# Kernel optimization log

Measured on AMD Instinct MI355X. Metric: run time of the kernel, lower is better.

The kernel has to match this reference:

```python
import jax, jax.numpy as jnp
import numpy as np

KSIZE = 3  # kernel_size (stride=1, dilation=1, groups=1, reduction_ratio=1)
BN_EPS = 1e-3  # keras BatchNormalization default epsilon


def setup_inputs() -> dict:
    key = jax.random.key(0)
    k0, k1, k2 = jax.random.split(key, 3)
    B, H, W, C = 8, 128, 128, 64
    x = jax.random.normal(k0, (B, H, W, C), jnp.float32)
    w1 = jax.random.normal(k1, (C, C), jnp.float32) * 0.05      # 1x1 conv C -> C//rr
    b1 = jnp.zeros((C,), jnp.float32)
    gamma = jnp.ones((C,), jnp.float32)
    beta = jnp.zeros((C,), jnp.float32)
    bn_mean = jnp.zeros((C,), jnp.float32)
    bn_var = jnp.ones((C,), jnp.float32)
    w2 = jax.random.normal(k2, (C, KSIZE * KSIZE), jnp.float32) * 0.05  # 1x1 conv -> K*K*G
    b2 = jnp.zeros((KSIZE * KSIZE,), jnp.float32)
    return dict(x=x, w1=w1, b1=b1, gamma=gamma, beta=beta,
                bn_mean=bn_mean, bn_var=bn_var, w2=w2, b2=b2)


def _extract_patches(x, k):
    # tf.image.extract_patches, SAME padding, stride 1, rate 1.
    # Returns (B, H, W, k*k, C) with patch index row-major over (di, dj).
    B, H, W, C = x.shape
    pad = k - 1
    pt = pad // 2
    xp = jnp.pad(x, ((0, 0), (pt, pad - pt), (pt, pad - pt), (0, 0)))
    shifts = [xp[:, i:i + H, j:j + W, :] for i in range(k) for j in range(k)]
    return jnp.stack(shifts, axis=3)


def reference(x, w1, b1, gamma, beta, bn_mean, bn_var, w2, b2):
    B, H, W, C = x.shape
    # kernel generation: 1x1 conv -> BN (inference stats) -> ReLU -> 1x1 conv
    h = jnp.einsum('bhwc,cd->bhwd', x, w1) + b1
    h = (h - bn_mean) * jax.lax.rsqrt(bn_var + BN_EPS) * gamma + beta
    h = jax.nn.relu(h)
    kern = jnp.einsum('bhwc,ck->bhwk', h, w2) + b2        # (B,H,W,K*K)
    # patch extraction + spatially-varying multiply-reduce over K*K
    patches = _extract_patches(x, KSIZE)                   # (B,H,W,K*K,C)
    out = jnp.einsum('bhwkc,bhwk->bhwc', patches, kern)    # (B,H,W,C)
    kernel = kern[..., None, None]                         # (B,H,W,K*K,1,G=1) as in tf reshape
    return out, kernel
```

## Files before the change

kernel.cpp:

```cpp
#include <hip/hip_runtime.h>

typedef unsigned int uint;
typedef unsigned short ushort_t;
typedef __attribute__((ext_vector_type(8))) short short8v;
typedef __attribute__((ext_vector_type(4))) float f32x4;

#define BATCH 8
#define HH 128
#define WW 128
#define CC 64
#define NPIX (BATCH * HH * WW)
#define KK 9
#define BN_EPS 1e-3f

__device__ __forceinline__ uint f2bfbits(float f) {
    uint u = __float_as_uint(f);
    return (u + 0x7fffu + ((u >> 16) & 1u)) >> 16;
}
__device__ __forceinline__ float bflo(uint u) { return __uint_as_float(u << 16); }
__device__ __forceinline__ float bfhi(uint u) { return __uint_as_float(u & 0xffff0000u); }

__global__ void setup_kernel(const float* __restrict__ w1,
                             const float* __restrict__ b1,
                             const float* __restrict__ gamma,
                             const float* __restrict__ beta,
                             const float* __restrict__ bn_mean,
                             const float* __restrict__ bn_var,
                             const float* __restrict__ w2,
                             const float* __restrict__ b2,
                             ushort_t* __restrict__ w1b,
                             ushort_t* __restrict__ w2bT,
                             float* __restrict__ scalef,
                             float* __restrict__ biasf,
                             float* __restrict__ b2f)
{
    int t = blockIdx.x * blockDim.x + threadIdx.x;
    int nt = gridDim.x * blockDim.x;
    for (int idx = t; idx < CC * CC; idx += nt) {
        int d = idx >> 6, c = idx & 63;
        w1b[idx] = (ushort_t)f2bfbits(w1[c * CC + d]);
    }
    for (int idx = t; idx < 16 * CC; idx += nt) {
        int k = idx >> 6, d = idx & 63;
        w2bT[idx] = (k < KK) ? (ushort_t)f2bfbits(w2[d * KK + k]) : (ushort_t)0;
    }
    if (t < CC) {
        float s = gamma[t] * rsqrtf(bn_var[t] + BN_EPS);
        scalef[t] = s;
        biasf[t] = (b1[t] - bn_mean[t]) * s + beta[t];
    }
    if (t < KK) b2f[t] = b2[t];
}

__global__ __launch_bounds__(256) void invol_fused(
    const float* __restrict__ x,
    const ushort_t* __restrict__ w1b,
    const ushort_t* __restrict__ w2bT,
    const float* __restrict__ scalef,
    const float* __restrict__ biasf,
    const float* __restrict__ b2f,
    float* __restrict__ out,
    float* __restrict__ kout)
{
    __shared__ ushort_t xrow[3][66][72];
    __shared__ ushort_t w1L[64][72];
    __shared__ ushort_t w2L[16][72];
    __shared__ ushort_t hL[4][16][72];
    __shared__ float    kS[64][12];

    const int t = threadIdx.x;
    const int w = __builtin_amdgcn_readfirstlane(t >> 6);
    const int l = t & 63;
    const int lq = l >> 4, lr = l & 15;
    int bid = blockIdx.x;
    bid = (bid & 7) * 256 + (bid >> 3);
    const int p0 = bid * 64;

    const int b  = p0 >> 14;
    const int i  = (p0 >> 7) & 127;
    const int j0 = p0 & 127;

#pragma unroll
    for (int r = 0; r < 3; ++r) {
        const int ir = min(max(i + r - 1, 0), HH - 1);
        const float* rowp = x + ((size_t)b * HH + ir) * WW * CC;
#pragma unroll
        for (int s = 0; s < 4; ++s) {
            int u = t + s * 256;
            int slot = u >> 4, c4 = u & 15;
            int jj = min(max(j0 + slot - 1, 0), WW - 1);
            float4 v = *(const float4*)(rowp + (size_t)jj * CC + c4 * 4);
            uint2 pk;
            pk.x = f2bfbits(v.x) | (f2bfbits(v.y) << 16);
            pk.y = f2bfbits(v.z) | (f2bfbits(v.w) << 16);
            *(uint2*)(&xrow[r][slot][c4 * 4]) = pk;
        }
        if (t < 32) {
            int u = t + 1024;
            int slot = u >> 4, c4 = u & 15;
            int jj = min(max(j0 + slot - 1, 0), WW - 1);
            float4 v = *(const float4*)(rowp + (size_t)jj * CC + c4 * 4);
            uint2 pk;
            pk.x = f2bfbits(v.x) | (f2bfbits(v.y) << 16);
            pk.y = f2bfbits(v.z) | (f2bfbits(v.w) << 16);
            *(uint2*)(&xrow[r][slot][c4 * 4]) = pk;
        }
    }
#pragma unroll
    for (int s = 0; s < 2; ++s) {
        int u = t + s * 256;
        int row = u >> 3, seg = u & 7;
        uint4 v = *(const uint4*)(w1b + row * CC + seg * 8);
        *(uint4*)(&w1L[row][seg * 8]) = v;
    }
    if (t < 128) {
        int row = t >> 3, seg = t & 7;
        uint4 v = *(const uint4*)(w2bT + row * CC + seg * 8);
        *(uint4*)(&w2L[row][seg * 8]) = v;
    }
    __syncthreads();

    {
        short8v af[2];
#pragma unroll
        for (int ks = 0; ks < 2; ++ks)
            af[ks] = *(const short8v*)(&xrow[1][w * 16 + lr + 1][ks * 32 + lq * 8]);

        f32x4 acc[4];
#pragma unroll
        for (int n = 0; n < 4; ++n) acc[n] = (f32x4){0.f, 0.f, 0.f, 0.f};
#pragma unroll
        for (int ks = 0; ks < 2; ++ks)
#pragma unroll
            for (int n = 0; n < 4; ++n) {
                short8v bf = *(const short8v*)(&w1L[n * 16 + lr][ks * 32 + lq * 8]);
                acc[n] = __builtin_amdgcn_mfma_f32_16x16x32_bf16(af[ks], bf, acc[n], 0, 0, 0);
            }
#pragma unroll
        for (int n = 0; n < 4; ++n) {
            const int d = n * 16 + lr;
            const float s = scalef[d], bb = biasf[d];
#pragma unroll
            for (int r = 0; r < 4; ++r) {
                float hv = fmaxf(fmaf(acc[n][r], s, bb), 0.f);
                hL[w][lq * 4 + r][d] = (ushort_t)f2bfbits(hv);
            }
        }
    }

    {
        f32x4 acc2 = (f32x4){0.f, 0.f, 0.f, 0.f};
#pragma unroll
        for (int ks = 0; ks < 2; ++ks) {
            short8v a2  = *(const short8v*)(&hL[w][lr][ks * 32 + lq * 8]);
            short8v b2v = *(const short8v*)(&w2L[lr][ks * 32 + lq * 8]);
            acc2 = __builtin_amdgcn_mfma_f32_16x16x32_bf16(a2, b2v, acc2, 0, 0, 0);
        }
        if (lr < KK) {
            const float bk = b2f[lr];
#pragma unroll
            for (int r = 0; r < 4; ++r)
                kS[w * 16 + lq * 4 + r][lr] = acc2[r] + bk;
        }
    }
    {
        float* kbase = kout + (size_t)(p0 + w * 16) * KK;
        if (l < 36) {
            float v[4];
#pragma unroll
            for (int e = 0; e < 4; ++e) {
                int f = l * 4 + e;
                v[e] = kS[w * 16 + f / KK][f % KK];
            }
            *(f32x4*)(kbase + l * 4) = (f32x4){v[0], v[1], v[2], v[3]};
        }
    }

    {
        float* obase = out + (size_t)(p0 + w * 16) * CC;
#pragma unroll
        for (int r = 0; r < 4; ++r) {
            const int flat = r * 64 + l;
            const int pxo = flat >> 4;
            const int g = flat & 15;
            const int pix = w * 16 + pxo;
            float a0 = 0.f, a1 = 0.f, a2 = 0.f, a3 = 0.f;
#pragma unroll
            for (int ti = 0; ti < 3; ++ti) {
                const int ii = i + ti - 1;
                if (ii < 0 || ii >= HH) continue;
#pragma unroll
                for (int tj = 0; tj < 3; ++tj) {
                    int jj = j0 + pix + tj - 1;
                    bool valid = (jj >= 0) && (jj < WW);
                    float kv = valid ? kS[pix][ti * 3 + tj] : 0.f;
                    uint2 u = *(const uint2*)(&xrow[ti][pix + tj][g * 4]);
                    a0 = fmaf(kv, bflo(u.x), a0);
                    a1 = fmaf(kv, bfhi(u.x), a1);
                    a2 = fmaf(kv, bflo(u.y), a2);
                    a3 = fmaf(kv, bfhi(u.y), a3);
                }
            }
            *(f32x4*)(obase + (size_t)flat * 4) = (f32x4){a0, a1, a2, a3};
        }
    }
}

extern "C" void kernel_launch(void* const* d_in, const int* in_sizes, int n_in,
                              void* d_out, int out_size, void* d_ws, size_t ws_size,
                              hipStream_t stream) {
    const float* x       = (const float*)d_in[0];
    const float* w1      = (const float*)d_in[1];
    const float* b1      = (const float*)d_in[2];
    const float* gamma   = (const float*)d_in[3];
    const float* beta    = (const float*)d_in[4];
    const float* bn_mean = (const float*)d_in[5];
    const float* bn_var  = (const float*)d_in[6];
    const float* w2      = (const float*)d_in[7];
    const float* b2      = (const float*)d_in[8];

    ushort_t* w1b  = (ushort_t*)d_ws;
    ushort_t* w2bT = w1b + CC * CC;
    float* scalef  = (float*)(w2bT + 16 * CC);
    float* biasf   = scalef + CC;
    float* b2f     = biasf + CC;

    float* out  = (float*)d_out;
    float* kout = out + (size_t)NPIX * CC;

    hipLaunchKernelGGL(setup_kernel, dim3(20), dim3(256), 0, stream,
                       w1, b1, gamma, beta, bn_mean, bn_var, w2, b2,
                       w1b, w2bT, scalef, biasf, b2f);

    hipLaunchKernelGGL(invol_fused, dim3(NPIX / 64), dim3(256), 0, stream,
                       x, w1b, w2bT, scalef, biasf, b2f, out, kout);
}
```

Before: 31.93 us.

## Process four rows per block with LDS row ring buffer and register prefetch

```diff
diff --git a/kernel.cpp b/kernel.cpp
--- a/kernel.cpp
+++ b/kernel.cpp
@@ -12,6 +12,8 @@
 #define NPIX (BATCH * HH * WW)
 #define KK 9
 #define BN_EPS 1e-3f
+#define ROWS 4
+#define NBLK (NPIX / (64 * ROWS))
 
 __device__ __forceinline__ uint f2bfbits(float f) {
     uint u = __float_as_uint(f);
@@ -62,7 +64,7 @@
     float* __restrict__ out,
     float* __restrict__ kout)
 {
-    __shared__ ushort_t xrow[3][66][72];
+    __shared__ ushort_t xrow[4][66][72];
     __shared__ ushort_t w1L[64][72];
     __shared__ ushort_t w2L[16][72];
     __shared__ ushort_t hL[4][16][72];
@@ -73,37 +75,56 @@
     const int l = t & 63;
     const int lq = l >> 4, lr = l & 15;
     int bid = blockIdx.x;
-    bid = (bid & 7) * 256 + (bid >> 3);
-    const int p0 = bid * 64;
-
-    const int b  = p0 >> 14;
-    const int i  = (p0 >> 7) & 127;
-    const int j0 = p0 & 127;
-
-#pragma unroll
-    for (int r = 0; r < 3; ++r) {
-        const int ir = min(max(i + r - 1, 0), HH - 1);
-        const float* rowp = x + ((size_t)b * HH + ir) * WW * CC;
+    bid = (bid & 7) * (NBLK / 8) + (bid >> 3);
+
+    const int jhalf = bid & 1;
+    const int grp = (bid >> 1) & 31;
+    const int b = bid >> 6;
+    const int i0 = grp * ROWS;
+    const int j0 = jhalf * 64;
+
+    auto stage_row_to_regs = [&](int ro, float4* sv) {
+        const float* rowp = x + ((size_t)b * HH + min(max(ro, 0), HH - 1)) * WW * CC;
 #pragma unroll
         for (int s = 0; s < 4; ++s) {
             int u = t + s * 256;
             int slot = u >> 4, c4 = u & 15;
             int jj = min(max(j0 + slot - 1, 0), WW - 1);
-            float4 v = *(const float4*)(rowp + (size_t)jj * CC + c4 * 4);
-            uint2 pk;
-            pk.x = f2bfbits(v.x) | (f2bfbits(v.y) << 16);
-            pk.y = f2bfbits(v.z) | (f2bfbits(v.w) << 16);
-            *(uint2*)(&xrow[r][slot][c4 * 4]) = pk;
+            sv[s] = *(const float4*)(rowp + (size_t)jj * CC + c4 * 4);
         }
         if (t < 32) {
             int u = t + 1024;
             int slot = u >> 4, c4 = u & 15;
             int jj = min(max(j0 + slot - 1, 0), WW - 1);
-            float4 v = *(const float4*)(rowp + (size_t)jj * CC + c4 * 4);
+            sv[4] = *(const float4*)(rowp + (size_t)jj * CC + c4 * 4);
+        }
+    };
+    auto write_row_to_lds = [&](int ringslot, const float4* sv) {
+#pragma unroll
+        for (int s = 0; s < 4; ++s) {
+            int u = t + s * 256;
+            int slot = u >> 4, c4 = u & 15;
             uint2 pk;
-            pk.x = f2bfbits(v.x) | (f2bfbits(v.y) << 16);
-            pk.y = f2bfbits(v.z) | (f2bfbits(v.w) << 16);
-            *(uint2*)(&xrow[r][slot][c4 * 4]) = pk;
+            pk.x = f2bfbits(sv[s].x) | (f2bfbits(sv[s].y) << 16);
+            pk.y = f2bfbits(sv[s].z) | (f2bfbits(sv[s].w) << 16);
+            *(uint2*)(&xrow[ringslot][slot][c4 * 4]) = pk;
+        }
+        if (t < 32) {
+            int u = t + 1024;
+            int slot = u >> 4, c4 = u & 15;
+            uint2 pk;
+            pk.x = f2bfbits(sv[4].x) | (f2bfbits(sv[4].y) << 16);
+            pk.y = f2bfbits(sv[4].z) | (f2bfbits(sv[4].w) << 16);
+            *(uint2*)(&xrow[ringslot][slot][c4 * 4]) = pk;
+        }
+    };
+
+    {
+        float4 sv[5];
+#pragma unroll
+        for (int r = 0; r < 3; ++r) {
+            stage_row_to_regs(i0 - 1 + r, sv);
+            write_row_to_lds(r, sv);
         }
     }
 #pragma unroll
@@ -120,88 +141,104 @@
     }
     __syncthreads();
 
-    {
-        short8v af[2];
-#pragma unroll
-        for (int ks = 0; ks < 2; ++ks)
-            af[ks] = *(const short8v*)(&xrow[1][w * 16 + lr + 1][ks * 32 + lq * 8]);
-
-        f32x4 acc[4];
-#pragma unroll
-        for (int n = 0; n < 4; ++n) acc[n] = (f32x4){0.f, 0.f, 0.f, 0.f};
-#pragma unroll
-        for (int ks = 0; ks < 2; ++ks)
+#pragma unroll
+    for (int r = 0; r < ROWS; ++r) {
+        const int i = i0 + r;
+        const int p0 = ((b * HH + i) * WW) + j0;
+        const int sTop = r & 3, sMid = (r + 1) & 3, sBot = (r + 2) & 3, sNew = (r + 3) & 3;
+
+        float4 sv[5];
+        if (r < ROWS - 1) stage_row_to_regs(i0 + r + 2, sv);
+
+        {
+            short8v af[2];
+#pragma unroll
+            for (int ks = 0; ks < 2; ++ks)
+                af[ks] = *(const short8v*)(&xrow[sMid][w * 16 + lr + 1][ks * 32 + lq * 8]);
+
+            f32x4 acc[4];
+#pragma unroll
+            for (int n = 0; n < 4; ++n) acc[n] = (f32x4){0.f, 0.f, 0.f, 0.f};
+#pragma unroll
+            for (int ks = 0; ks < 2; ++ks)
+#pragma unroll
+                for (int n = 0; n < 4; ++n) {
+                    short8v bf = *(const short8v*)(&w1L[n * 16 + lr][ks * 32 + lq * 8]);
+                    acc[n] = __builtin_amdgcn_mfma_f32_16x16x32_bf16(af[ks], bf, acc[n], 0, 0, 0);
+                }
 #pragma unroll
             for (int n = 0; n < 4; ++n) {
-                short8v bf = *(const short8v*)(&w1L[n * 16 + lr][ks * 32 + lq * 8]);
-                acc[n] = __builtin_amdgcn_mfma_f32_16x16x32_bf16(af[ks], bf, acc[n], 0, 0, 0);
-            }
-#pragma unroll
-        for (int n = 0; n < 4; ++n) {
-            const int d = n * 16 + lr;
-            const float s = scalef[d], bb = biasf[d];
-#pragma unroll
-            for (int r = 0; r < 4; ++r) {
-                float hv = fmaxf(fmaf(acc[n][r], s, bb), 0.f);
-                hL[w][lq * 4 + r][d] = (ushort_t)f2bfbits(hv);
-            }
-        }
-    }
-
-    {
-        f32x4 acc2 = (f32x4){0.f, 0.f, 0.f, 0.f};
-#pragma unroll
-        for (int ks = 0; ks < 2; ++ks) {
-            short8v a2  = *(const short8v*)(&hL[w][lr][ks * 32 + lq * 8]);
-            short8v b2v = *(const short8v*)(&w2L[lr][ks * 32 + lq * 8]);
-            acc2 = __builtin_amdgcn_mfma_f32_16x16x32_bf16(a2, b2v, acc2, 0, 0, 0);
-        }
-        if (lr < KK) {
-            const float bk = b2f[lr];
-#pragma unroll
-            for (int r = 0; r < 4; ++r)
-                kS[w * 16 + lq * 4 + r][lr] = acc2[r] + bk;
-        }
-    }
-    {
-        float* kbase = kout + (size_t)(p0 + w * 16) * KK;
-        if (l < 36) {
-            float v[4];
-#pragma unroll
-            for (int e = 0; e < 4; ++e) {
-                int f = l * 4 + e;
-                v[e] = kS[w * 16 + f / KK][f % KK];
-            }
-            *(f32x4*)(kbase + l * 4) = (f32x4){v[0], v[1], v[2], v[3]};
-        }
-    }
-
-    {
-        float* obase = out + (size_t)(p0 + w * 16) * CC;
-#pragma unroll
-        for (int r = 0; r < 4; ++r) {
-            const int flat = r * 64 + l;
-            const int pxo = flat >> 4;
-            const int g = flat & 15;
-            const int pix = w * 16 + pxo;
-            float a0 = 0.f, a1 = 0.f, a2 = 0.f, a3 = 0.f;
-#pragma unroll
-            for (int ti = 0; ti < 3; ++ti) {
-                const int ii = i + ti - 1;
-                if (ii < 0 || ii >= HH) continue;
-#pragma unroll
-                for (int tj = 0; tj < 3; ++tj) {
-                    int jj = j0 + pix + tj - 1;
-                    bool valid = (jj >= 0) && (jj < WW);
-                    float kv = valid ? kS[pix][ti * 3 + tj] : 0.f;
-                    uint2 u = *(const uint2*)(&xrow[ti][pix + tj][g * 4]);
-                    a0 = fmaf(kv, bflo(u.x), a0);
-                    a1 = fmaf(kv, bfhi(u.x), a1);
-                    a2 = fmaf(kv, bflo(u.y), a2);
-                    a3 = fmaf(kv, bfhi(u.y), a3);
-                }
-            }
-            *(f32x4*)(obase + (size_t)flat * 4) = (f32x4){a0, a1, a2, a3};
+                const int d = n * 16 + lr;
+                const float s = scalef[d], bb = biasf[d];
+#pragma unroll
+                for (int q = 0; q < 4; ++q) {
+                    float hv = fmaxf(fmaf(acc[n][q], s, bb), 0.f);
+                    hL[w][lq * 4 + q][d] = (ushort_t)f2bfbits(hv);
+                }
+            }
+        }
+
+        {
+            f32x4 acc2 = (f32x4){0.f, 0.f, 0.f, 0.f};
+#pragma unroll
+            for (int ks = 0; ks < 2; ++ks) {
+                short8v a2  = *(const short8v*)(&hL[w][lr][ks * 32 + lq * 8]);
+                short8v b2v = *(const short8v*)(&w2L[lr][ks * 32 + lq * 8]);
+                acc2 = __builtin_amdgcn_mfma_f32_16x16x32_bf16(a2, b2v, acc2, 0, 0, 0);
+            }
+            if (lr < KK) {
+                const float bk = b2f[lr];
+#pragma unroll
+                for (int q = 0; q < 4; ++q)
+                    kS[w * 16 + lq * 4 + q][lr] = acc2[q] + bk;
+            }
+        }
+        {
+            float* kbase = kout + (size_t)(p0 + w * 16) * KK;
+            if (l < 36) {
+                float v[4];
+#pragma unroll
+                for (int e = 0; e < 4; ++e) {
+                    int f = l * 4 + e;
+                    v[e] = kS[w * 16 + f / KK][f % KK];
+                }
+                *(f32x4*)(kbase + l * 4) = (f32x4){v[0], v[1], v[2], v[3]};
+            }
+        }
+
+        {
+            float* obase = out + (size_t)(p0 + w * 16) * CC;
+#pragma unroll
+            for (int rr = 0; rr < 4; ++rr) {
+                const int flat = rr * 64 + l;
+                const int pxo = flat >> 4;
+                const int g = flat & 15;
+                const int pix = w * 16 + pxo;
+                float a0 = 0.f, a1 = 0.f, a2 = 0.f, a3 = 0.f;
+#pragma unroll
+                for (int ti = 0; ti < 3; ++ti) {
+                    const int ii = i + ti - 1;
+                    if (ii < 0 || ii >= HH) continue;
+                    const int sl = (ti == 0) ? sTop : (ti == 1) ? sMid : sBot;
+#pragma unroll
+                    for (int tj = 0; tj < 3; ++tj) {
+                        int jj = j0 + pix + tj - 1;
+                        bool valid = (jj >= 0) && (jj < WW);
+                        float kv = valid ? kS[pix][ti * 3 + tj] : 0.f;
+                        uint2 u = *(const uint2*)(&xrow[sl][pix + tj][g * 4]);
+                        a0 = fmaf(kv, bflo(u.x), a0);
+                        a1 = fmaf(kv, bfhi(u.x), a1);
+                        a2 = fmaf(kv, bflo(u.y), a2);
+                        a3 = fmaf(kv, bfhi(u.y), a3);
+                    }
+                }
+                *(f32x4*)(obase + (size_t)flat * 4) = (f32x4){a0, a1, a2, a3};
+            }
+        }
+
+        if (r < ROWS - 1) {
+            write_row_to_lds(sNew, sv);
+            __syncthreads();
         }
     }
 }
@@ -232,6 +269,6 @@
                        w1, b1, gamma, beta, bn_mean, bn_var, w2, b2,
                        w1b, w2bT, scalef, biasf, b2f);
 
-    hipLaunchKernelGGL(invol_fused, dim3(NPIX / 64), dim3(256), 0, stream,
+    hipLaunchKernelGGL(invol_fused, dim3(NBLK), dim3(256), 0, stream,
                        x, w1b, w2bT, scalef, biasf, b2f, out, kout);
 }
```

Measured after the change: 28.86 us. -9.6%, faster.
